# Kernel optimization log

Measured on AMD Instinct MI355X. Metric: run time of the kernel, lower is better.

Reference implementation:

```python
import jax, jax.numpy as jnp
import numpy as np

B, L, D, H = 2, 2048, 2048, 16
Dh = D // H
EPS = 1e-6
THETA = 500000.0


def _rope_cos_sin(dh, seq_len):
    # matches init_rope: per-head dim, theta=500000
    inv_freqs = 1.0 / (THETA ** (jnp.arange(0, dh, 2, dtype=jnp.float32) / dh))  # [Dh/2]
    t = jnp.arange(seq_len, dtype=jnp.float32)
    freqs = jnp.outer(t, inv_freqs)  # [L, Dh/2]
    return jnp.cos(freqs), jnp.sin(freqs)


def _apply_rope(x, cos, sin):
    # x: [B,L,H,Dh]; cos/sin: [L,Dh/2]
    xr = x.reshape(*x.shape[:-1], -1, 2)  # [B,L,H,Dh/2,2]
    c = cos[None, :, None, :]
    s = sin[None, :, None, :]
    rot = jnp.stack([xr[..., 0] * c - xr[..., 1] * s,
                     xr[..., 1] * c + xr[..., 0] * s], axis=-1)
    return rot.reshape(x.shape)


def setup_inputs() -> dict:
    key = jax.random.key(0)
    ks = jax.random.split(key, 5)
    std = 0.02
    x = jax.random.normal(ks[0], (B, L, D), dtype=jnp.float32)
    Wq = std * jax.random.normal(ks[1], (D, H, Dh), dtype=jnp.float32)
    Wk = std * jax.random.normal(ks[2], (D, H, Dh), dtype=jnp.float32)
    Wv = std * jax.random.normal(ks[3], (D, H, Dh), dtype=jnp.float32)
    Wout = (std / jnp.sqrt(2.0 * 24)) * jax.random.normal(ks[4], (D, D), dtype=jnp.float32)
    attn_scale = jnp.asarray(jnp.log2(float(L) ** 2 - float(L)), dtype=jnp.float32)
    return {"x": x, "Wq": Wq, "Wk": Wk, "Wv": Wv, "Wout": Wout, "attn_scale": attn_scale}


def reference(x, Wq, Wk, Wv, Wout, attn_scale):
    cos, sin = _rope_cos_sin(Dh, L)
    q = jnp.einsum('bld,dhk->blhk', x, Wq)  # [B,L,H,Dh]
    k = jnp.einsum('bld,dhk->blhk', x, Wk)
    v = jnp.einsum('bld,dhk->blhk', x, Wv)
    q = _apply_rope(q, cos, sin)
    k = _apply_rope(k, cos, sin)
    # QK L2 normalization
    q = q / (jnp.linalg.norm(q, axis=-1, keepdims=True) + EPS)
    k = k / (jnp.linalg.norm(k, axis=-1, keepdims=True) + EPS)
    att = jnp.einsum('bqhd,bkhd->bhqk', q, k)  # [B,H,L,L]
    mask = jnp.tril(jnp.ones((1, 1, L, L), dtype=jnp.bool_))
    neg_inf = jnp.finfo(jnp.float32).min
    att = jnp.where(mask, att, neg_inf)
    att = attn_scale * att
    att = jax.nn.softmax(att, axis=-1)
    out = jnp.einsum('bhqk,bkhd->bqhd', att, v)  # [B,L,H,Dh]
    out = out.reshape(B, L, D)
    return jnp.einsum('bld,de->ble', out, Wout)
```

## Files before the change

kernel.cpp:

```cpp
#include <hip/hip_runtime.h>
#include <hip/hip_fp16.h>

#define B_ 2
#define L_ 2048
#define D_ 2048
#define H_ 16
#define DH_ 128

typedef _Float16 f16;
typedef _Float16 f16x8 __attribute__((ext_vector_type(8)));
typedef _Float16 f16x4 __attribute__((ext_vector_type(4)));
typedef _Float16 f16x2 __attribute__((ext_vector_type(2)));
typedef float f32x4 __attribute__((ext_vector_type(4)));

__device__ __forceinline__ void gload_lds16(const void* g, void* l) {
  __builtin_amdgcn_global_load_lds(
      (__attribute__((address_space(1))) void*)(void*)g,
      (__attribute__((address_space(3))) void*)l, 16, 0, 0);
}

template <int N>
__device__ __forceinline__ void waitcnt_vm() {
  if constexpr (N == 0) asm volatile("s_waitcnt vmcnt(0)" ::: "memory");
  else if constexpr (N == 4) asm volatile("s_waitcnt vmcnt(4)" ::: "memory");
  else if constexpr (N == 6) asm volatile("s_waitcnt vmcnt(6)" ::: "memory");
  else if constexpr (N == 8) asm volatile("s_waitcnt vmcnt(8)" ::: "memory");
}

__device__ __forceinline__ float rmax16(float v) {
  v = fmaxf(v, __shfl_xor(v, 1));
  v = fmaxf(v, __shfl_xor(v, 2));
  v = fmaxf(v, __shfl_xor(v, 4));
  v = fmaxf(v, __shfl_xor(v, 8));
  return v;
}
__device__ __forceinline__ float rsum16(float v) {
  v += __shfl_xor(v, 1);
  v += __shfl_xor(v, 2);
  v += __shfl_xor(v, 4);
  v += __shfl_xor(v, 8);
  return v;
}

__global__ __launch_bounds__(256) void k_cast(const float* __restrict__ in,
                                              f16* __restrict__ out, int n8) {
  int i = blockIdx.x * blockDim.x + threadIdx.x;
  if (i >= n8) return;
  const float4* p = (const float4*)in + (size_t)i * 2;
  float4 a = p[0], b = p[1];
  f16x8 o;
  o[0] = (f16)a.x; o[1] = (f16)a.y; o[2] = (f16)a.z; o[3] = (f16)a.w;
  o[4] = (f16)b.x; o[5] = (f16)b.y; o[6] = (f16)b.z; o[7] = (f16)b.w;
  *((f16x8*)out + i) = o;
}

__global__ __launch_bounds__(256) void k_transpose4(
    const float* __restrict__ W0, const float* __restrict__ W1,
    const float* __restrict__ W2, const float* __restrict__ W3,
    f16* __restrict__ T0, f16* __restrict__ T1, f16* __restrict__ T2,
    f16* __restrict__ T3) {
  int z = blockIdx.z;
  const float* src = (z == 0) ? W0 : (z == 1) ? W1 : (z == 2) ? W2 : W3;
  f16* dst = (z == 0) ? T0 : (z == 1) ? T1 : (z == 2) ? T2 : T3;
  __shared__ float tile[32][33];
  int tx = threadIdx.x, ty = threadIdx.y;
  int x = blockIdx.x * 32 + tx;
  int y0 = blockIdx.y * 32;
#pragma unroll
  for (int i = 0; i < 4; ++i)
    tile[ty + i * 8][tx] = src[(size_t)(y0 + ty + i * 8) * 2048 + x];
  __syncthreads();
  int ox = y0 + tx;
  int oy0 = blockIdx.x * 32;
#pragma unroll
  for (int i = 0; i < 4; ++i)
    dst[(size_t)(oy0 + ty + i * 8) * 2048 + ox] = (f16)tile[tx][ty + i * 8];
}

template <int NL>
__device__ __forceinline__ void stage_slot(const char* __restrict__ src,
                                           char* dst, int tid) {
#pragma unroll
  for (int j = 0; j < NL; ++j) {
    int ci = j * 512 + tid;
    int row = ci >> 3;
    int sc = (ci & 7) ^ (row & 7);
    gload_lds16(src + (size_t)row * 4096 + sc * 16, dst + ci * 16);
  }
}

__global__ __launch_bounds__(512, 2) void k_gemm8_qkv(
    const f16* __restrict__ x16, const f16* __restrict__ WT ,
    f16* __restrict__ qh, f16* __restrict__ kh, f16* __restrict__ vTo) {
  constexpr int ABYTES = 128 * 128;
  constexpr int BUFB = ABYTES + 384 * 128;
  constexpr int nt = 32;
  __shared__ alignas(16) char lds[2 * BUFB];

  const int pb = blockIdx.x;
  const int lgc = (pb & 7) * 64 + (pb >> 3);
  const int m0 = (lgc >> 4) * 128;
  const int n0 = (lgc & 15) * 384;

  const int tid = threadIdx.x;
  const int lane = tid & 63, w = tid >> 6;
  const int wr = w >> 2, wc = w & 3;
  const int li = lane & 15, lg = lane >> 4;

  const char* Ab = (const char*)x16 + (size_t)m0 * 4096;
  const char* Bb = (const char*)WT + (size_t)n0 * 4096;

  f32x4 acc[4][6] = {};

#pragma unroll
  for (int t = 0; t < 2; ++t) {
    char* bA = lds + t * BUFB;
    stage_slot<2>(Ab + t * 128, bA, tid);
    stage_slot<6>(Bb + t * 128, bA + ABYTES, tid);
  }
  waitcnt_vm<8>();
  __builtin_amdgcn_s_barrier();

  const int sx = (li & 7);

#pragma unroll 1
  for (int u = 0; u < nt; ++u) {
    const int c = u & 1;
    char* bufA = lds + c * BUFB;
    char* bufB = bufA + ABYTES;
    char* oA = lds + (c ^ 1) * BUFB;
    f16x8 af[4][2], bf[6][2];

#pragma unroll
    for (int mr = 0; mr < 4; ++mr) {
      int rb = (wr * 64 + mr * 16 + li) * 128;
      af[mr][0] = *(const f16x8*)(bufA + rb + ((lg ^ sx) << 4));
      af[mr][1] = *(const f16x8*)(bufA + rb + (((4 + lg) ^ sx) << 4));
    }
#pragma unroll
    for (int nc = 0; nc < 2; ++nc) {
      int rb = (wc * 96 + nc * 16 + li) * 128;
      bf[nc][0] = *(const f16x8*)(bufB + rb + ((lg ^ sx) << 4));
      bf[nc][1] = *(const f16x8*)(bufB + rb + (((4 + lg) ^ sx) << 4));
    }
    if (u >= 1 && u + 1 < nt) stage_slot<2>(Ab + (size_t)(u + 1) * 128, oA, tid);
    __builtin_amdgcn_s_barrier();
    asm volatile("s_waitcnt lgkmcnt(0)" ::: "memory");
    __builtin_amdgcn_sched_barrier(0);
    __builtin_amdgcn_s_setprio(1);
#pragma unroll
    for (int mr = 0; mr < 4; ++mr)
#pragma unroll
      for (int nc = 0; nc < 2; ++nc) {
        acc[mr][nc] = __builtin_amdgcn_mfma_f32_16x16x32_f16(af[mr][0], bf[nc][0],
                                                             acc[mr][nc], 0, 0, 0);
        acc[mr][nc] = __builtin_amdgcn_mfma_f32_16x16x32_f16(af[mr][1], bf[nc][1],
                                                             acc[mr][nc], 0, 0, 0);
      }
    __builtin_amdgcn_s_setprio(0);
    __builtin_amdgcn_s_barrier();

#pragma unroll
    for (int nc = 2; nc < 6; ++nc) {
      int rb = (wc * 96 + nc * 16 + li) * 128;
      bf[nc][0] = *(const f16x8*)(bufB + rb + ((lg ^ sx) << 4));
      bf[nc][1] = *(const f16x8*)(bufB + rb + (((4 + lg) ^ sx) << 4));
    }
    __builtin_amdgcn_s_barrier();
    asm volatile("s_waitcnt lgkmcnt(0)" ::: "memory");
    __builtin_amdgcn_sched_barrier(0);
    __builtin_amdgcn_s_setprio(1);
#pragma unroll
    for (int mr = 0; mr < 4; ++mr)
#pragma unroll
      for (int nc = 2; nc < 4; ++nc) {
        acc[mr][nc] = __builtin_amdgcn_mfma_f32_16x16x32_f16(af[mr][0], bf[nc][0],
                                                             acc[mr][nc], 0, 0, 0);
        acc[mr][nc] = __builtin_amdgcn_mfma_f32_16x16x32_f16(af[mr][1], bf[nc][1],
                                                             acc[mr][nc], 0, 0, 0);
      }
    __builtin_amdgcn_s_setprio(0);
    __builtin_amdgcn_s_barrier();

    if (u + 2 < nt) stage_slot<6>(Bb + (size_t)(u + 2) * 128, bufB, tid);
    if (u + 2 < nt) waitcnt_vm<6>();
    else if (u + 1 < nt) waitcnt_vm<0>();
    __builtin_amdgcn_s_barrier();
    __builtin_amdgcn_sched_barrier(0);
    __builtin_amdgcn_s_setprio(1);
#pragma unroll
    for (int mr = 0; mr < 4; ++mr)
#pragma unroll
      for (int nc = 4; nc < 6; ++nc) {
        acc[mr][nc] = __builtin_amdgcn_mfma_f32_16x16x32_f16(af[mr][0], bf[nc][0],
                                                             acc[mr][nc], 0, 0, 0);
        acc[mr][nc] = __builtin_amdgcn_mfma_f32_16x16x32_f16(af[mr][1], bf[nc][1],
                                                             acc[mr][nc], 0, 0, 0);
      }
    __builtin_amdgcn_s_setprio(0);
    __builtin_amdgcn_s_barrier();
  }

#pragma unroll
  for (int mr = 0; mr < 4; ++mr) {
    int mb = m0 + wr * 64 + mr * 16 + lg * 4;
    int b = mb >> 11, l = mb & 2047;
#pragma unroll
    for (int nc = 0; nc < 6; ++nc) {
      int n = n0 + wc * 96 + nc * 16 + li;
      int z = n >> 11, n2 = n & 2047;
      int h = n2 >> 7, dh = n2 & 127;
      if (z < 2) {
        f16* out = (z == 0) ? qh : kh;
#pragma unroll
        for (int r2 = 0; r2 < 4; ++r2) {
          int m = mb + r2;
          out[(((size_t)(b * 16 + h) * 2048 + (m & 2047)) << 7) + dh] =
              (f16)acc[mr][nc][r2];
        }
      } else {
        f16x4 v4;
#pragma unroll
        for (int r2 = 0; r2 < 4; ++r2) v4[r2] = (f16)acc[mr][nc][r2];
        *(f16x4*)(vTo + ((size_t)(b * 16 + h) * 128 + dh) * 2048 + l) = v4;
      }
    }
  }
}

template <int BM>
__device__ __forceinline__ void gemm8_core(const f16* __restrict__ A,
                                           const f16* __restrict__ BT,
                                           char* lds, int m0, int n0,
                                           f32x4 (&acc)[BM / 32][4]) {
  constexpr int WRS = BM / 2;
  constexpr int MR = BM / 32;
  constexpr int MPP = MR / 4;
  constexpr int ALOADS = BM / 128;
  constexpr int LPT = 2 * ALOADS + 4;
  constexpr int ABYTES = BM * 128;
  constexpr int BUFB = ABYTES + 32768;
  constexpr int nt = 32;

  const int tid = threadIdx.x;
  const int lane = tid & 63, w = tid >> 6;
  const int wr = w >> 2, wc = w & 3;
  const int li = lane & 15, lg = lane >> 4;

  const char* Ab = (const char*)A + (size_t)m0 * 4096;
  const char* Bb = (const char*)BT + (size_t)n0 * 4096;

  const int aoff0 = (wr * WRS + li) * 128 + ((lg) ^ (li & 7)) * 16;
  const int aoff1 = (wr * WRS + li) * 128 + ((4 + lg) ^ (li & 7)) * 16;
  const int boff0 = (wc * 64 + li) * 128 + ((lg) ^ (li & 7)) * 16;
  const int boff1 = (wc * 64 + li) * 128 + ((4 + lg) ^ (li & 7)) * 16;

#pragma unroll
  for (int t = 0; t < 2; ++t) {
    char* bA = lds + t * BUFB;
    stage_slot<ALOADS>(Ab + t * 128, bA, tid);
    stage_slot<ALOADS>(Ab + (size_t)WRS * 4096 + t * 128, bA + (size_t)WRS * 128, tid);
    stage_slot<2>(Bb + t * 128, bA + ABYTES, tid);
    stage_slot<2>(Bb + (size_t)128 * 4096 + t * 128, bA + ABYTES + 128 * 128, tid);
  }
  waitcnt_vm<LPT>();
  __builtin_amdgcn_s_barrier();

#pragma unroll 1
  for (int u = 0; u < nt; ++u) {
    const int c = u & 1;
    char* bufA = lds + c * BUFB;
    char* bufB = bufA + ABYTES;
    char* oA = lds + (c ^ 1) * BUFB;
    f16x8 bf[4][2];
#pragma unroll
    for (int p = 0; p < 4; ++p) {
      f16x8 af[MPP][2];
#pragma unroll
      for (int i = 0; i < MPP; ++i) {
        af[i][0] = *(const f16x8*)(bufA + aoff0 + (p * MPP + i) * 2048);
        af[i][1] = *(const f16x8*)(bufA + aoff1 + (p * MPP + i) * 2048);
      }
      if (p == 0) {
#pragma unroll
        for (int nc = 0; nc < 4; ++nc) {
          bf[nc][0] = *(const f16x8*)(bufB + boff0 + nc * 2048);
          bf[nc][1] = *(const f16x8*)(bufB + boff1 + nc * 2048);
        }
      }
      if (p == 0 && u >= 1 && u + 1 < nt)
        stage_slot<ALOADS>(Ab + (size_t)(u + 1) * 128, oA, tid);
      if (p == 1 && u >= 1 && u + 1 < nt)
        stage_slot<ALOADS>(Ab + (size_t)WRS * 4096 + (size_t)(u + 1) * 128,
                           oA + (size_t)WRS * 128, tid);
      if (p == 2 && u + 2 < nt)
        stage_slot<2>(Bb + (size_t)(u + 2) * 128, bufB, tid);
      if (p == 3 && u + 2 < nt)
        stage_slot<2>(Bb + (size_t)128 * 4096 + (size_t)(u + 2) * 128,
                      bufB + 128 * 128, tid);
      if (p == 3) {
        if (u + 2 < nt) waitcnt_vm<4>();
        else if (u + 1 < nt) waitcnt_vm<0>();
      }
      __builtin_amdgcn_s_barrier();
      asm volatile("s_waitcnt lgkmcnt(0)" ::: "memory");
      __builtin_amdgcn_sched_barrier(0);
      __builtin_amdgcn_s_setprio(1);
#pragma unroll
      for (int i = 0; i < MPP; ++i)
#pragma unroll
        for (int nc = 0; nc < 4; ++nc) {
          acc[p * MPP + i][nc] = __builtin_amdgcn_mfma_f32_16x16x32_f16(
              af[i][0], bf[nc][0], acc[p * MPP + i][nc], 0, 0, 0);
          acc[p * MPP + i][nc] = __builtin_amdgcn_mfma_f32_16x16x32_f16(
              af[i][1], bf[nc][1], acc[p * MPP + i][nc], 0, 0, 0);
        }
      __builtin_amdgcn_s_setprio(0);
      __builtin_amdgcn_s_barrier();
    }
  }
}

__global__ __launch_bounds__(512, 2) void k_gemm8_out(
    const f16* __restrict__ A, const f16* __restrict__ WoutT,
    float* __restrict__ out) {
  __shared__ alignas(16) char lds[2 * (128 * 128 + 32768)];
  const int pb = blockIdx.x;
  const int lgc = (pb & 7) * 32 + (pb >> 3);
  const int m0 = (lgc >> 3) * 128, n0 = (lgc & 7) * 256;
  f32x4 acc[4][4] = {};
  gemm8_core<128>(A, WoutT, lds, m0, n0, acc);

  const int lane = threadIdx.x & 63, w = threadIdx.x >> 6;
  const int wr = w >> 2, wc = w & 3, li = lane & 15, lg = lane >> 4;
#pragma unroll
  for (int mr = 0; mr < 4; ++mr) {
#pragma unroll
    for (int nc = 0; nc < 4; ++nc) {
      int n = n0 + wc * 64 + nc * 16 + li;
#pragma unroll
      for (int r2 = 0; r2 < 4; ++r2) {
        int m = m0 + wr * 64 + mr * 16 + lg * 4 + r2;
        out[(size_t)m * 2048 + n] = acc[mr][nc][r2];
      }
    }
  }
}

__global__ __launch_bounds__(256) void k_rope_norm(f16* __restrict__ qh,
                                                   f16* __restrict__ kh) {
  int gid = blockIdx.x * 4 + (threadIdx.x >> 6);
  int lane = threadIdx.x & 63;
  int which = gid >> 16;
  int r = gid & 65535;
  int l = r & 2047;
  f16* base = (which ? kh : qh) + (size_t)r * 128;
  f16x2 xv = *(f16x2*)(base + lane * 2);
  float x0 = (float)xv[0], x1 = (float)xv[1];
  float invf = exp2f(-(float)lane * 0.29580575889569f);
  float ang = (float)l * invf;
  float s, c;
  sincosf(ang, &s, &c);
  float y0 = x0 * c - x1 * s;
  float y1 = x1 * c + x0 * s;
  float ss = y0 * y0 + y1 * y1;
  ss += __shfl_xor(ss, 1);  ss += __shfl_xor(ss, 2);
  ss += __shfl_xor(ss, 4);  ss += __shfl_xor(ss, 8);
  ss += __shfl_xor(ss, 16); ss += __shfl_xor(ss, 32);
  float inv = 1.0f / (sqrtf(ss) + 1e-6f);
  f16x2 o;
  o[0] = (f16)(y0 * inv);
  o[1] = (f16)(y1 * inv);
  *(f16x2*)(base + lane * 2) = o;
}

__global__ __launch_bounds__(256) void k_flash(
    const f16* __restrict__ qh, const f16* __restrict__ kh,
    const f16* __restrict__ vT, f16* __restrict__ attO,
    const float* __restrict__ ascale_p) {
  const int bh = blockIdx.y;
  const int tid = threadIdx.x, lane = tid & 63, w = tid >> 6;
  const int li = lane & 15, lg = lane >> 4;
  const float csc = ascale_p[0] * 1.44269504088896f;
  const float thr = 8.0f / csc;

  __shared__ alignas(16) f16 Ks[2][64 * 128];
  __shared__ alignas(16) f16 Vs[2][128 * 64];
  __shared__ alignas(16) f16 Ps[4][16 * 72];

  const f16* qb = qh + (size_t)bh * 2048 * 128;
  const char* kbB = (const char*)(kh + (size_t)bh * 2048 * 128);
  const char* vbB = (const char*)(vT + (size_t)bh * 128 * 2048);
  const int b = bh >> 4, h = bh & 15;
  const int sx = li & 7;

  auto stage_tile = [&](int kt, int bsel) {
    char* Kd = (char*)Ks[bsel];
    char* Vd = (char*)Vs[bsel];
    const char* ksrc = kbB + (size_t)kt * 64 * 256;
    const char* vsrc = vbB + (size_t)kt * 128;
#pragma unroll
    for (int j = 0; j < 4; ++j) {
      int ci = j * 256 + tid;
      int row = ci >> 4, sc = (ci & 15) ^ (row & 7);
      gload_lds16(ksrc + (size_t)row * 256 + sc * 16, Kd + ci * 16);
      int row2 = ci >> 3, sc2 = (ci & 7) ^ (row2 & 7);
      gload_lds16(vsrc + (size_t)row2 * 4096 + sc2 * 16, Vd + ci * 16);
    }
  };

#pragma unroll 1
  for (int ti = 0; ti < 2; ++ti) {
    const int t = ti ? (31 - (int)blockIdx.x) : (int)blockIdx.x;
    const int qw = t * 64 + w * 16;

    f16x8 Qr[4];
#pragma unroll
    for (int ks = 0; ks < 4; ++ks)
      Qr[ks] = *(const f16x8*)(qb + (size_t)(qw + li) * 128 + ks * 32 + lg * 8);

    f32x4 Oa[8] = {};
    float mrow[4], lrow[4];
#pragma unroll
    for (int r = 0; r < 4; ++r) { mrow[r] = -1e30f; lrow[r] = 0.0f; }

    stage_tile(0, 0);
    waitcnt_vm<0>();
    __syncthreads();

#pragma unroll 1
    for (int kt = 0; kt <= t; ++kt) {
      const int c = kt & 1;
      if (kt + 1 <= t) stage_tile(kt + 1, c ^ 1);
      const char* Kb = (const char*)Ks[c];
      const char* Vb = (const char*)Vs[c];

      f32x4 Sa[4] = {};
      __builtin_amdgcn_s_setprio(1);
#pragma unroll
      for (int ks = 0; ks < 4; ++ks) {
        f16x8 kf4[4];
#pragma unroll
        for (int kf = 0; kf < 4; ++kf) {
          int cc = (ks * 4 + lg) ^ sx;
          kf4[kf] = *(const f16x8*)(Kb + (kf * 16 + li) * 256 + cc * 16);
        }
#pragma unroll
        for (int kf = 0; kf < 4; ++kf)
          Sa[kf] = __builtin_amdgcn_mfma_f32_16x16x32_f16(Qr[ks], kf4[kf],
                                                          Sa[kf], 0, 0, 0);
      }
      __builtin_amdgcn_s_setprio(0);

      if (kt == t) {
#pragma unroll
        for (int kf = 0; kf < 4; ++kf)
#pragma unroll
          for (int r = 0; r < 4; ++r) {
            int qq = qw + lg * 4 + r;
            int kk = t * 64 + kf * 16 + li;
            if (kk > qq) Sa[kf][r] = -1e30f;
          }
      }

      float vmax[4];
      bool need = false;
#pragma unroll
      for (int r = 0; r < 4; ++r) {
        float v = fmaxf(fmaxf(Sa[0][r], Sa[1][r]), fmaxf(Sa[2][r], Sa[3][r]));
        v = rmax16(v);
        vmax[r] = v;
        need |= (v > mrow[r] + thr);
      }
      if (__any(need)) {
#pragma unroll
        for (int r = 0; r < 4; ++r) {
          float mnew = fmaxf(mrow[r], vmax[r]);
          float sc = exp2f(csc * (mrow[r] - mnew));
          mrow[r] = mnew;
          lrow[r] *= sc;
#pragma unroll
          for (int df = 0; df < 8; ++df) Oa[df][r] *= sc;
        }
      }
#pragma unroll
      for (int r = 0; r < 4; ++r) {
        float rs = 0.0f;
#pragma unroll
        for (int kf = 0; kf < 4; ++kf) {
          float p = exp2f(csc * (Sa[kf][r] - mrow[r]));
          Sa[kf][r] = p;
          rs += p;
        }
        rs = rsum16(rs);
        lrow[r] += rs;
      }

      f16* Pw = &Ps[w][0];
#pragma unroll
      for (int kf = 0; kf < 4; ++kf)
#pragma unroll
        for (int r = 0; r < 4; ++r)
          Pw[(lg * 4 + r) * 72 + kf * 16 + li] = (f16)Sa[kf][r];
      asm volatile("s_waitcnt lgkmcnt(0)" ::: "memory");
      __builtin_amdgcn_sched_barrier(0);
      __builtin_amdgcn_s_setprio(1);
#pragma unroll
      for (int k2 = 0; k2 < 2; ++k2) {
        f16x8 pa, vfr[8];
        pa = *(const f16x8*)(Pw + li * 72 + k2 * 32 + lg * 8);
#pragma unroll
        for (int df = 0; df < 8; ++df) {
          int cc = (k2 * 4 + lg) ^ sx;
          vfr[df] = *(const f16x8*)(Vb + (df * 16 + li) * 128 + cc * 16);
        }
#pragma unroll
        for (int df = 0; df < 8; ++df)
          Oa[df] = __builtin_amdgcn_mfma_f32_16x16x32_f16(pa, vfr[df],
                                                          Oa[df], 0, 0, 0);
      }
      __builtin_amdgcn_s_setprio(0);
      waitcnt_vm<0>();
      __syncthreads();
    }

#pragma unroll
    for (int r = 0; r < 4; ++r) {
      float inv = 1.0f / lrow[r];
      int q = qw + lg * 4 + r;
      f16* orow = attO + (size_t)(b * 2048 + q) * 2048 + h * 128;
#pragma unroll
      for (int df = 0; df < 8; ++df)
        orow[df * 16 + li] = (f16)(Oa[df][r] * inv);
    }
    __syncthreads();
  }
}

extern "C" void kernel_launch(void* const* d_in, const int* in_sizes, int n_in,
                              void* d_out, int out_size, void* d_ws, size_t ws_size,
                              hipStream_t stream) {
  (void)in_sizes; (void)n_in; (void)out_size; (void)ws_size;
  const float* x = (const float*)d_in[0];
  const float* Wq = (const float*)d_in[1];
  const float* Wk = (const float*)d_in[2];
  const float* Wv = (const float*)d_in[3];
  const float* Wout = (const float*)d_in[4];
  const float* ascale = (const float*)d_in[5];

  char* ws = (char*)d_ws;
  f16* x16 = (f16*)(ws);
  f16* WoutT = (f16*)(ws + (16ull << 20));
  f16* WqT = (f16*)(ws + (24ull << 20));
  f16* WkT = (f16*)(ws + (32ull << 20));
  f16* WvT = (f16*)(ws + (40ull << 20));
  f16* qh = (f16*)(ws + (48ull << 20));
  f16* kh = (f16*)(ws + (64ull << 20));
  f16* vT = (f16*)(ws + (80ull << 20));
  f16* attO = (f16*)(ws + (24ull << 20));

  k_cast<<<dim3(4096), dim3(256), 0, stream>>>(x, x16, 1048576);
  k_transpose4<<<dim3(64, 64, 4), dim3(32, 8), 0, stream>>>(Wq, Wk, Wv, Wout,
                                                            WqT, WkT, WvT, WoutT);
  k_gemm8_qkv<<<dim3(512), dim3(512), 0, stream>>>(x16, WqT, qh, kh, vT);
  k_rope_norm<<<dim3(32768), dim3(256), 0, stream>>>(qh, kh);
  k_flash<<<dim3(16, 32), dim3(256), 0, stream>>>(qh, kh, vT, attO, ascale);
  k_gemm8_out<<<dim3(256), dim3(512), 0, stream>>>(attO, WoutT, (float*)d_out);
}
```

Before: 423.9 us.

## Load K/V fragments directly from global in flash kernel; remap QKV GEMM tiles

The flash attention kernel stops staging K and V tiles into double-buffered LDS. Each wave now reads its MFMA fragments straight from global memory, which removes the async LDS copies, the wait counters and the block-wide barriers. The price is that all four waves issue redundant global loads for the same K/V data and rely on L1/L2 to absorb them, with less latency hiding. The QKV GEMM also swaps its block-to-tile mapping so that consecutive blocks walk M instead of N, which changes L2 reuse of the weights and activations.

```diff
diff --git a/kernel.cpp b/kernel.cpp
--- a/kernel.cpp
+++ b/kernel.cpp
@@ -99,8 +99,8 @@
 
   const int pb = blockIdx.x;
   const int lgc = (pb & 7) * 64 + (pb >> 3);
-  const int m0 = (lgc >> 4) * 128;
-  const int n0 = (lgc & 15) * 384;
+  const int m0 = (lgc & 31) * 128;
+  const int n0 = (lgc >> 5) * 384;
 
   const int tid = threadIdx.x;
   const int lane = tid & 63, w = tid >> 6;
@@ -384,30 +384,12 @@
   const float csc = ascale_p[0] * 1.44269504088896f;
   const float thr = 8.0f / csc;
 
-  __shared__ alignas(16) f16 Ks[2][64 * 128];
-  __shared__ alignas(16) f16 Vs[2][128 * 64];
   __shared__ alignas(16) f16 Ps[4][16 * 72];
 
   const f16* qb = qh + (size_t)bh * 2048 * 128;
-  const char* kbB = (const char*)(kh + (size_t)bh * 2048 * 128);
-  const char* vbB = (const char*)(vT + (size_t)bh * 128 * 2048);
+  const f16* kb = kh + (size_t)bh * 2048 * 128;
+  const f16* vb = vT + (size_t)bh * 128 * 2048;
   const int b = bh >> 4, h = bh & 15;
-  const int sx = li & 7;
-
-  auto stage_tile = [&](int kt, int bsel) {
-    char* Kd = (char*)Ks[bsel];
-    char* Vd = (char*)Vs[bsel];
-    const char* ksrc = kbB + (size_t)kt * 64 * 256;
-    const char* vsrc = vbB + (size_t)kt * 128;
-#pragma unroll
-    for (int j = 0; j < 4; ++j) {
-      int ci = j * 256 + tid;
-      int row = ci >> 4, sc = (ci & 15) ^ (row & 7);
-      gload_lds16(ksrc + (size_t)row * 256 + sc * 16, Kd + ci * 16);
-      int row2 = ci >> 3, sc2 = (ci & 7) ^ (row2 & 7);
-      gload_lds16(vsrc + (size_t)row2 * 4096 + sc2 * 16, Vd + ci * 16);
-    }
-  };
 
 #pragma unroll 1
   for (int ti = 0; ti < 2; ++ti) {
@@ -424,16 +406,10 @@
 #pragma unroll
     for (int r = 0; r < 4; ++r) { mrow[r] = -1e30f; lrow[r] = 0.0f; }
 
-    stage_tile(0, 0);
-    waitcnt_vm<0>();
-    __syncthreads();
-
 #pragma unroll 1
     for (int kt = 0; kt <= t; ++kt) {
-      const int c = kt & 1;
-      if (kt + 1 <= t) stage_tile(kt + 1, c ^ 1);
-      const char* Kb = (const char*)Ks[c];
-      const char* Vb = (const char*)Vs[c];
+      const f16* kbase = kb + (size_t)kt * 64 * 128;
+      const f16* vbase = vb + kt * 64;
 
       f32x4 Sa[4] = {};
       __builtin_amdgcn_s_setprio(1);
@@ -441,10 +417,8 @@
       for (int ks = 0; ks < 4; ++ks) {
         f16x8 kf4[4];
 #pragma unroll
-        for (int kf = 0; kf < 4; ++kf) {
-          int cc = (ks * 4 + lg) ^ sx;
-          kf4[kf] = *(const f16x8*)(Kb + (kf * 16 + li) * 256 + cc * 16);
-        }
+        for (int kf = 0; kf < 4; ++kf)
+          kf4[kf] = *(const f16x8*)(kbase + (kf * 16 + li) * 128 + ks * 32 + lg * 8);
 #pragma unroll
         for (int kf = 0; kf < 4; ++kf)
           Sa[kf] = __builtin_amdgcn_mfma_f32_16x16x32_f16(Qr[ks], kf4[kf],
@@ -510,18 +484,15 @@
         f16x8 pa, vfr[8];
         pa = *(const f16x8*)(Pw + li * 72 + k2 * 32 + lg * 8);
 #pragma unroll
-        for (int df = 0; df < 8; ++df) {
-          int cc = (k2 * 4 + lg) ^ sx;
-          vfr[df] = *(const f16x8*)(Vb + (df * 16 + li) * 128 + cc * 16);
-        }
+        for (int df = 0; df < 8; ++df)
+          vfr[df] = *(const f16x8*)(vbase + (size_t)(df * 16 + li) * 2048 +
+                                    k2 * 32 + lg * 8);
 #pragma unroll
         for (int df = 0; df < 8; ++df)
           Oa[df] = __builtin_amdgcn_mfma_f32_16x16x32_f16(pa, vfr[df],
                                                           Oa[df], 0, 0, 0);
       }
       __builtin_amdgcn_s_setprio(0);
-      waitcnt_vm<0>();
-      __syncthreads();
     }
 
 #pragma unroll
@@ -533,7 +504,6 @@
       for (int df = 0; df < 8; ++df)
         orow[df * 16 + li] = (f16)(Oa[df][r] * inv);
     }
-    __syncthreads();
   }
 }
 
```

After: 563.0 us. +32.8%, slower.
